# Performance work log

Hardware: AMD Instinct MI355X
Metric: run time of the kernel (lower is better)

Reference implementation:

```python
import jax, jax.numpy as jnp
import numpy as np


def setup_inputs() -> dict:
    key = jax.random.key(0)
    k1, k2 = jax.random.split(key)
    B, H, N, C = 8, 8, 2048, 64
    x = jax.random.normal(k1, (B, H, N, C), dtype=jnp.float32)
    # torch nn.Linear(dim, 3*dim) weight layout: [3C, C]
    W_qkv = jax.random.normal(k2, (3 * C, C), dtype=jnp.float32) * (C ** -0.5)
    return {"x": x, "W_qkv": W_qkv}


def reference(x, W_qkv):
    B, H, N, C = x.shape
    scale = C ** -0.5
    # fused qkv projection: x @ W^T, then split
    qkv = jnp.einsum('bhnc,dc->bhnd', x, W_qkv)  # [B,H,N,3C]
    q, k, v = jnp.split(qkv, 3, axis=-1)
    # full N x N score matrix (matches the naive original)
    attn = jnp.einsum('bhnc,bhmc->bhnm', q, k) * scale
    attn = jax.nn.softmax(attn, axis=-1)
    out = jnp.einsum('bhnm,bhmc->bhnc', attn, v)  # [B,H,N,C]
    # head-mixing shuffle: reshape(B,H,N,H,C//H).transpose(1,3).reshape(B,H,N,C)
    out = out.reshape(B, H, N, H, C // H)
    out = out.transpose(0, 3, 2, 1, 4)
    return out.reshape(B, H, N, C)
```

## Files before the change

### kernel.cpp

```cpp
#include <hip/hip_runtime.h>
#include <math.h>

#define BH    64
#define NSEQ  2048
#define CDIM  64
#define WSTR  72

typedef unsigned short ushort_t;
typedef __attribute__((ext_vector_type(8))) short short8;
typedef __attribute__((ext_vector_type(4))) float float4v;

__device__ __forceinline__ ushort_t f32_to_bf16_rne(float x) {
  unsigned int u = __float_as_uint(x);
  u += 0x7fffu + ((u >> 16) & 1u);
  return (ushort_t)(u >> 16);
}

__device__ __forceinline__ unsigned int pk2(float a, float b) {
  return ((__float_as_uint(a) + 0x8000u) >> 16) |
         ((__float_as_uint(b) + 0x8000u) & 0xffff0000u);
}

__device__ __forceinline__ void glds16(const ushort_t* g, ushort_t* l) {
  __builtin_amdgcn_global_load_lds(
      (const __attribute__((address_space(1))) void*)g,
      (__attribute__((address_space(3))) void*)l, 16, 0, 0);
}

__global__ __launch_bounds__(256) void qkv_proj_mfma(
    const float* __restrict__ x, const float* __restrict__ w,
    ushort_t* __restrict__ q, ushort_t* __restrict__ k,
    ushort_t* __restrict__ vt) {
  __shared__ ushort_t Wb[192 * WSTR];
  const int t = threadIdx.x;
  const int lane = t & 63, wv = t >> 6;
  const int quad = lane >> 4, l16 = lane & 15;
  const long rowbase = (long)blockIdx.x * 128;
  const int head  = (int)(rowbase >> 11);
  const int nbase = (int)(rowbase & 2047);

  for (int u = t; u < 1536; u += 256) {
    const int d = u >> 3, o8 = (u & 7) * 8;
    const float sc = (d < 64) ? 0.1803368801111244f : 1.0f;
    const float4 f0 = *reinterpret_cast<const float4*>(w + d * 64 + o8);
    const float4 f1 = *reinterpret_cast<const float4*>(w + d * 64 + o8 + 4);
    ushort_t tmp[8] __attribute__((aligned(16)));
    tmp[0] = f32_to_bf16_rne(f0.x * sc); tmp[1] = f32_to_bf16_rne(f0.y * sc);
    tmp[2] = f32_to_bf16_rne(f0.z * sc); tmp[3] = f32_to_bf16_rne(f0.w * sc);
    tmp[4] = f32_to_bf16_rne(f1.x * sc); tmp[5] = f32_to_bf16_rne(f1.y * sc);
    tmp[6] = f32_to_bf16_rne(f1.z * sc); tmp[7] = f32_to_bf16_rne(f1.w * sc);
    *reinterpret_cast<uint4*>(&Wb[d * WSTR + o8]) = *reinterpret_cast<const uint4*>(tmp);
  }
  __syncthreads();

  short8 xf[2][2];
#pragma unroll
  for (int tm = 0; tm < 2; ++tm)
#pragma unroll
    for (int kb = 0; kb < 2; ++kb) {
      const float* xp = x + (rowbase + wv * 32 + tm * 16 + l16) * 64 + kb * 32 + quad * 8;
      const float4 f0 = *reinterpret_cast<const float4*>(xp);
      const float4 f1 = *reinterpret_cast<const float4*>(xp + 4);
      ushort_t tmp[8] __attribute__((aligned(16)));
      tmp[0] = f32_to_bf16_rne(f0.x); tmp[1] = f32_to_bf16_rne(f0.y);
      tmp[2] = f32_to_bf16_rne(f0.z); tmp[3] = f32_to_bf16_rne(f0.w);
      tmp[4] = f32_to_bf16_rne(f1.x); tmp[5] = f32_to_bf16_rne(f1.y);
      tmp[6] = f32_to_bf16_rne(f1.z); tmp[7] = f32_to_bf16_rne(f1.w);
      xf[tm][kb] = *reinterpret_cast<const short8*>(tmp);
    }

  float4v aqk[8][2];
  float4v av[2][4];
#pragma unroll
  for (int nt = 0; nt < 8; ++nt)
#pragma unroll
    for (int tm = 0; tm < 2; ++tm)
#pragma unroll
      for (int r = 0; r < 4; ++r) aqk[nt][tm][r] = 0.f;
#pragma unroll
  for (int tm = 0; tm < 2; ++tm)
#pragma unroll
    for (int nt = 0; nt < 4; ++nt)
#pragma unroll
      for (int r = 0; r < 4; ++r) av[tm][nt][r] = 0.f;

#pragma unroll
  for (int kb = 0; kb < 2; ++kb) {
#pragma unroll
    for (int nt = 0; nt < 8; ++nt) {
      const short8 wf = *reinterpret_cast<const short8*>(
          &Wb[(nt * 16 + l16) * WSTR + kb * 32 + quad * 8]);
      aqk[nt][0] = __builtin_amdgcn_mfma_f32_16x16x32_bf16(wf, xf[0][kb], aqk[nt][0], 0, 0, 0);
      aqk[nt][1] = __builtin_amdgcn_mfma_f32_16x16x32_bf16(wf, xf[1][kb], aqk[nt][1], 0, 0, 0);
    }
#pragma unroll
    for (int nt = 0; nt < 4; ++nt) {
      const short8 wfv = *reinterpret_cast<const short8*>(
          &Wb[((128 + nt * 16) + l16) * WSTR + kb * 32 + quad * 8]);
      av[0][nt] = __builtin_amdgcn_mfma_f32_16x16x32_bf16(xf[0][kb], wfv, av[0][nt], 0, 0, 0);
      av[1][nt] = __builtin_amdgcn_mfma_f32_16x16x32_bf16(xf[1][kb], wfv, av[1][nt], 0, 0, 0);
    }
  }

#pragma unroll
  for (int tm = 0; tm < 2; ++tm) {
    const long row = rowbase + wv * 32 + tm * 16 + l16;
#pragma unroll
    for (int nt = 0; nt < 8; ++nt) {
      uint2 pk;
      pk.x = pk2(aqk[nt][tm][0], aqk[nt][tm][1]);
      pk.y = pk2(aqk[nt][tm][2], aqk[nt][tm][3]);
      if (nt < 4)
        *reinterpret_cast<uint2*>(q + row * 64 + nt * 16 + quad * 4) = pk;
      else
        *reinterpret_cast<uint2*>(k + row * 64 + (nt - 4) * 16 + quad * 4) = pk;
    }
  }
#pragma unroll
  for (int tm = 0; tm < 2; ++tm)
#pragma unroll
    for (int nt = 0; nt < 4; ++nt) {
      const int c = nt * 16 + l16;
      uint2 pk;
      pk.x = pk2(av[tm][nt][0], av[tm][nt][1]);
      pk.y = pk2(av[tm][nt][2], av[tm][nt][3]);
      *reinterpret_cast<uint2*>(vt + (long)head * (64 * 2048) + (long)c * 2048 +
                                nbase + wv * 32 + tm * 16 + quad * 4) = pk;
    }
}

__global__ __launch_bounds__(256, 2) void flash_attn_mfma(
    const ushort_t* __restrict__ q, const ushort_t* __restrict__ k,
    const ushort_t* __restrict__ vt, float* __restrict__ out) {
  __shared__ ushort_t Ks2[2][32 * 64];
  __shared__ ushort_t Vs2[2][64 * 32];
  __shared__ ushort_t Ps[256 * 32];
  const int t = threadIdx.x;
  const int lane = t & 63, w = t >> 6;
  const int quad = lane >> 4, l16 = lane & 15;
  const int id = blockIdx.x;
  const int qt = id >> 6;
  const int bh = ((id & 7) << 3) | ((id >> 3) & 7);
  const long hoff = (long)bh * NSEQ * CDIM;
  const ushort_t* qp  = q  + hoff + (long)qt * 256 * CDIM;
  const ushort_t* kp  = k  + hoff;
  const ushort_t* vtp = vt + hoff;

  short8 qf[4][2];
#pragma unroll
  for (int tm = 0; tm < 4; ++tm)
#pragma unroll
    for (int kb = 0; kb < 2; ++kb)
      qf[tm][kb] = *reinterpret_cast<const short8*>(
          qp + (w * 64 + tm * 16 + l16) * 64 + kb * 32 + quad * 8);

  float4v O[4][4];
  float rs[4];
#pragma unroll
  for (int tm = 0; tm < 4; ++tm) rs[tm] = 0.f;
#pragma unroll
  for (int ct = 0; ct < 4; ++ct)
#pragma unroll
    for (int tm = 0; tm < 4; ++tm)
#pragma unroll
      for (int r = 0; r < 4; ++r) O[ct][tm][r] = 0.f;

  const int krow = w * 8 + (lane >> 3);
  const int kchk = (lane & 7) ^ (lane >> 3);
  const int kdst = w * 8 * 64;
  const int vrow = w * 16 + (lane >> 2);
  const int vchk = (lane & 3) ^ ((lane >> 3) & 3);
  const int vdst = w * 16 * 32;
  const int pswz = (l16 >> 1) & 3;

  glds16(kp + (long)krow * 64 + kchk * 8, &Ks2[0][kdst]);
  glds16(vtp + (long)vrow * 2048 + vchk * 8, &Vs2[0][vdst]);

  for (int tile = 0; tile < NSEQ / 32; ++tile) {
    const int cur = tile & 1;
    __syncthreads();
    if (tile < NSEQ / 32 - 1) {
      const long nxt = tile + 1;
      glds16(kp + (nxt * 32 + krow) * 64 + kchk * 8, &Ks2[1 - cur][kdst]);
      glds16(vtp + (long)vrow * 2048 + nxt * 32 + vchk * 8, &Vs2[1 - cur][vdst]);
    }

    float4v s[2][4];
#pragma unroll
    for (int nt = 0; nt < 2; ++nt)
#pragma unroll
      for (int tm = 0; tm < 4; ++tm)
#pragma unroll
        for (int r = 0; r < 4; ++r) s[nt][tm][r] = 0.f;

#pragma unroll
    for (int kb = 0; kb < 2; ++kb) {
      short8 kf[2];
#pragma unroll
      for (int nt = 0; nt < 2; ++nt)
        kf[nt] = *reinterpret_cast<const short8*>(
            &Ks2[cur][(nt * 16 + l16) * 64 + (((kb * 4 + quad) ^ (l16 & 7)) * 8)]);
#pragma unroll
      for (int nt = 0; nt < 2; ++nt)
#pragma unroll
        for (int tm = 0; tm < 4; ++tm)
          s[nt][tm] = __builtin_amdgcn_mfma_f32_16x16x32_bf16(
              kf[nt], qf[tm][kb], s[nt][tm], 0, 0, 0);
    }

#pragma unroll
    for (int tm = 0; tm < 4; ++tm)
#pragma unroll
      for (int nt = 0; nt < 2; ++nt) {
        const float p0 = __builtin_amdgcn_exp2f(s[nt][tm][0]);
        const float p1 = __builtin_amdgcn_exp2f(s[nt][tm][1]);
        const float p2 = __builtin_amdgcn_exp2f(s[nt][tm][2]);
        const float p3 = __builtin_amdgcn_exp2f(s[nt][tm][3]);
        rs[tm] += (p0 + p1) + (p2 + p3);
        uint2 pk;
        pk.x = pk2(p0, p1);
        pk.y = pk2(p2, p3);
        *reinterpret_cast<uint2*>(
            &Ps[(w * 64 + tm * 16 + l16) * 32 +
                (((nt * 2 + (quad >> 1)) ^ pswz) * 8) + (quad & 1) * 4]) = pk;
      }

    {
      short8 pf[4], vf[4];
#pragma unroll
      for (int tm = 0; tm < 4; ++tm)
        pf[tm] = *reinterpret_cast<const short8*>(
            &Ps[(w * 64 + tm * 16 + l16) * 32 + ((quad ^ pswz) * 8)]);
#pragma unroll
      for (int ct = 0; ct < 4; ++ct)
        vf[ct] = *reinterpret_cast<const short8*>(
            &Vs2[cur][(ct * 16 + l16) * 32 + ((quad ^ pswz) * 8)]);
#pragma unroll
      for (int ct = 0; ct < 4; ++ct)
#pragma unroll
        for (int tm = 0; tm < 4; ++tm)
          O[ct][tm] = __builtin_amdgcn_mfma_f32_16x16x32_bf16(
              vf[ct], pf[tm], O[ct][tm], 0, 0, 0);
    }
  }

  const int bi = bh >> 3, h = bh & 7;
  float inv[4];
#pragma unroll
  for (int tm = 0; tm < 4; ++tm) {
    float l = rs[tm];
    l += __shfl_xor(l, 16, 64);
    l += __shfl_xor(l, 32, 64);
    inv[tm] = 1.f / l;
  }
#pragma unroll
  for (int ct = 0; ct < 4; ++ct)
#pragma unroll
    for (int tm = 0; tm < 4; ++tm) {
      const int n = qt * 256 + w * 64 + tm * 16 + l16;
      const int h2 = ct * 2 + (quad >> 1);
      const int c2b = (quad & 1) * 4;
      float4 v4;
      v4.x = O[ct][tm][0] * inv[tm]; v4.y = O[ct][tm][1] * inv[tm];
      v4.z = O[ct][tm][2] * inv[tm]; v4.w = O[ct][tm][3] * inv[tm];
      *reinterpret_cast<float4*>(
          &out[(((long)(bi * 8 + h2)) * NSEQ + n) * 64 + h * 8 + c2b]) = v4;
    }
}

extern "C" void kernel_launch(void* const* d_in, const int* in_sizes, int n_in,
                              void* d_out, int out_size, void* d_ws, size_t ws_size,
                              hipStream_t stream) {
  (void)in_sizes; (void)n_in; (void)out_size; (void)ws_size;
  const float* x = (const float*)d_in[0];
  const float* w = (const float*)d_in[1];
  float* out = (float*)d_out;

  ushort_t* qws  = (ushort_t*)d_ws;
  ushort_t* kws  = qws + (size_t)BH * NSEQ * CDIM;
  ushort_t* vtws = kws + (size_t)BH * NSEQ * CDIM;

  qkv_proj_mfma<<<(BH * NSEQ) / 128, 256, 0, stream>>>(x, w, qws, kws, vtws);
  flash_attn_mfma<<<512, 256, 0, stream>>>(qws, kws, vtws, out);
}
```

Baseline: 180.9 us.

## Split flash attention block across 8 waves and use hardware bf16 pack

The attention kernel now launches 512 threads per block, so each of 8 waves handles 32 query rows instead of 64. K and V tile loads are split so waves 0-3 load K and waves 4-7 load V. Per-wave accumulators shrink, which lowers register pressure and allows more waves per CU to hide latency. The bf16 packing of probabilities now uses the v_cvt_pk_bf16_f32 instruction instead of manual bit arithmetic. The trade-offs are more per-block barrier synchronisation and less reuse of each K/V fragment per MFMA issue.

```diff
diff --git a/kernel.cpp b/kernel.cpp
--- a/kernel.cpp
+++ b/kernel.cpp
@@ -19,6 +19,12 @@
 __device__ __forceinline__ unsigned int pk2(float a, float b) {
   return ((__float_as_uint(a) + 0x8000u) >> 16) |
          ((__float_as_uint(b) + 0x8000u) & 0xffff0000u);
+}
+
+__device__ __forceinline__ unsigned int cvtpk(float a, float b) {
+  unsigned int r;
+  asm("v_cvt_pk_bf16_f32 %0, %1, %2" : "=v"(r) : "v"(a), "v"(b));
+  return r;
 }
 
 __device__ __forceinline__ void glds16(const ushort_t* g, ushort_t* l) {
@@ -129,7 +135,7 @@
     }
 }
 
-__global__ __launch_bounds__(256, 2) void flash_attn_mfma(
+__global__ __launch_bounds__(512, 4) void flash_attn_mfma(
     const ushort_t* __restrict__ q, const ushort_t* __restrict__ k,
     const ushort_t* __restrict__ vt, float* __restrict__ out) {
   __shared__ ushort_t Ks2[2][32 * 64];
@@ -146,50 +152,51 @@
   const ushort_t* kp  = k  + hoff;
   const ushort_t* vtp = vt + hoff;
 
-  short8 qf[4][2];
-#pragma unroll
-  for (int tm = 0; tm < 4; ++tm)
+  short8 qf[2][2];
+#pragma unroll
+  for (int tm = 0; tm < 2; ++tm)
 #pragma unroll
     for (int kb = 0; kb < 2; ++kb)
       qf[tm][kb] = *reinterpret_cast<const short8*>(
-          qp + (w * 64 + tm * 16 + l16) * 64 + kb * 32 + quad * 8);
-
-  float4v O[4][4];
-  float rs[4];
-#pragma unroll
-  for (int tm = 0; tm < 4; ++tm) rs[tm] = 0.f;
+          qp + (w * 32 + tm * 16 + l16) * 64 + kb * 32 + quad * 8);
+
+  float4v O[4][2];
+  float rs[2];
+  rs[0] = 0.f; rs[1] = 0.f;
 #pragma unroll
   for (int ct = 0; ct < 4; ++ct)
 #pragma unroll
-    for (int tm = 0; tm < 4; ++tm)
+    for (int tm = 0; tm < 2; ++tm)
 #pragma unroll
       for (int r = 0; r < 4; ++r) O[ct][tm][r] = 0.f;
 
-  const int krow = w * 8 + (lane >> 3);
+  const int ws = w & 3;
+  const bool isK = (w < 4);
+  const int krow = ws * 8 + (lane >> 3);
   const int kchk = (lane & 7) ^ (lane >> 3);
-  const int kdst = w * 8 * 64;
-  const int vrow = w * 16 + (lane >> 2);
+  const int kdst = ws * 8 * 64;
+  const int vrow = ws * 16 + (lane >> 2);
   const int vchk = (lane & 3) ^ ((lane >> 3) & 3);
-  const int vdst = w * 16 * 32;
+  const int vdst = ws * 16 * 32;
   const int pswz = (l16 >> 1) & 3;
 
-  glds16(kp + (long)krow * 64 + kchk * 8, &Ks2[0][kdst]);
-  glds16(vtp + (long)vrow * 2048 + vchk * 8, &Vs2[0][vdst]);
+  if (isK) glds16(kp + (long)krow * 64 + kchk * 8, &Ks2[0][kdst]);
+  else     glds16(vtp + (long)vrow * 2048 + vchk * 8, &Vs2[0][vdst]);
 
   for (int tile = 0; tile < NSEQ / 32; ++tile) {
     const int cur = tile & 1;
     __syncthreads();
     if (tile < NSEQ / 32 - 1) {
       const long nxt = tile + 1;
-      glds16(kp + (nxt * 32 + krow) * 64 + kchk * 8, &Ks2[1 - cur][kdst]);
-      glds16(vtp + (long)vrow * 2048 + nxt * 32 + vchk * 8, &Vs2[1 - cur][vdst]);
-    }
-
-    float4v s[2][4];
+      if (isK) glds16(kp + (nxt * 32 + krow) * 64 + kchk * 8, &Ks2[1 - cur][kdst]);
+      else     glds16(vtp + (long)vrow * 2048 + nxt * 32 + vchk * 8, &Vs2[1 - cur][vdst]);
+    }
+
+    float4v s[2][2];
 #pragma unroll
     for (int nt = 0; nt < 2; ++nt)
 #pragma unroll
-      for (int tm = 0; tm < 4; ++tm)
+      for (int tm = 0; tm < 2; ++tm)
 #pragma unroll
         for (int r = 0; r < 4; ++r) s[nt][tm][r] = 0.f;
 
@@ -203,13 +210,13 @@
 #pragma unroll
       for (int nt = 0; nt < 2; ++nt)
 #pragma unroll
-        for (int tm = 0; tm < 4; ++tm)
+        for (int tm = 0; tm < 2; ++tm)
           s[nt][tm] = __builtin_amdgcn_mfma_f32_16x16x32_bf16(
               kf[nt], qf[tm][kb], s[nt][tm], 0, 0, 0);
     }
 
 #pragma unroll
-    for (int tm = 0; tm < 4; ++tm)
+    for (int tm = 0; tm < 2; ++tm)
 #pragma unroll
       for (int nt = 0; nt < 2; ++nt) {
         const float p0 = __builtin_amdgcn_exp2f(s[nt][tm][0]);
@@ -218,19 +225,19 @@
         const float p3 = __builtin_amdgcn_exp2f(s[nt][tm][3]);
         rs[tm] += (p0 + p1) + (p2 + p3);
         uint2 pk;
-        pk.x = pk2(p0, p1);
-        pk.y = pk2(p2, p3);
+        pk.x = cvtpk(p0, p1);
+        pk.y = cvtpk(p2, p3);
         *reinterpret_cast<uint2*>(
-            &Ps[(w * 64 + tm * 16 + l16) * 32 +
+            &Ps[(w * 32 + tm * 16 + l16) * 32 +
                 (((nt * 2 + (quad >> 1)) ^ pswz) * 8) + (quad & 1) * 4]) = pk;
       }
 
     {
-      short8 pf[4], vf[4];
-#pragma unroll
-      for (int tm = 0; tm < 4; ++tm)
+      short8 pf[2], vf[4];
+#pragma unroll
+      for (int tm = 0; tm < 2; ++tm)
         pf[tm] = *reinterpret_cast<const short8*>(
-            &Ps[(w * 64 + tm * 16 + l16) * 32 + ((quad ^ pswz) * 8)]);
+            &Ps[(w * 32 + tm * 16 + l16) * 32 + ((quad ^ pswz) * 8)]);
 #pragma unroll
       for (int ct = 0; ct < 4; ++ct)
         vf[ct] = *reinterpret_cast<const short8*>(
@@ -238,16 +245,16 @@
 #pragma unroll
       for (int ct = 0; ct < 4; ++ct)
 #pragma unroll
-        for (int tm = 0; tm < 4; ++tm)
+        for (int tm = 0; tm < 2; ++tm)
           O[ct][tm] = __builtin_amdgcn_mfma_f32_16x16x32_bf16(
               vf[ct], pf[tm], O[ct][tm], 0, 0, 0);
     }
   }
 
   const int bi = bh >> 3, h = bh & 7;
-  float inv[4];
-#pragma unroll
-  for (int tm = 0; tm < 4; ++tm) {
+  float inv[2];
+#pragma unroll
+  for (int tm = 0; tm < 2; ++tm) {
     float l = rs[tm];
     l += __shfl_xor(l, 16, 64);
     l += __shfl_xor(l, 32, 64);
@@ -256,8 +263,8 @@
 #pragma unroll
   for (int ct = 0; ct < 4; ++ct)
 #pragma unroll
-    for (int tm = 0; tm < 4; ++tm) {
-      const int n = qt * 256 + w * 64 + tm * 16 + l16;
+    for (int tm = 0; tm < 2; ++tm) {
+      const int n = qt * 256 + w * 32 + tm * 16 + l16;
       const int h2 = ct * 2 + (quad >> 1);
       const int c2b = (quad & 1) * 4;
       float4 v4;
@@ -281,5 +288,5 @@
   ushort_t* vtws = kws + (size_t)BH * NSEQ * CDIM;
 
   qkv_proj_mfma<<<(BH * NSEQ) / 128, 256, 0, stream>>>(x, w, qws, kws, vtws);
-  flash_attn_mfma<<<512, 256, 0, stream>>>(qws, kws, vtws, out);
-}
+  flash_attn_mfma<<<512, 512, 0, stream>>>(qws, kws, vtws, out);
+}
```

Result: faster. 171.2 us (-5.4%).
